# Optimization experiments

Hardware: AMD Instinct MI355X
Metric: run time of the kernel (lower is better)

Reference implementation:

```python
import jax, jax.numpy as jnp
import numpy as np

B, N, R, T, E, H, FE = 2, 512, 64, 128, 64, 8, 4
D = E // H  # head_dim = 8


def _layernorm(x, g, b):
    m = x.mean(-1, keepdims=True)
    v = ((x - m) ** 2).mean(-1, keepdims=True)
    return (x - m) / jnp.sqrt(v + 1e-5) * g + b


def _sattn(v, k, q, Wv, Wk, Wq, Wo, bo, mask):
    # v,k: (Bk,Nk,T,E); q: (Bq,Nq,T,E) with Bq possibly 1 (broadcast on batch)
    Bk, Nk, Tk, _ = v.shape
    Nq = q.shape[1]
    v = v.reshape(Bk, Nk, Tk, H, D) @ Wv
    k = k.reshape(Bk, Nk, Tk, H, D) @ Wk
    q = q.reshape(q.shape[0], Nq, Tk, H, D) @ Wq
    q = jnp.broadcast_to(q, (Bk, Nq, Tk, H, D))
    energy = jnp.einsum('bqthd,bkthd->bqkth', q, k)  # (B,Nq,Nk,T,H)
    if mask is not None:
        m = mask[None, :, :, None, None]
        energy = energy * m + (-1e8) * (1.0 - m)
    # note: non-standard softmax over the QUERY axis (dim=1), after scale+clamp
    att = jax.nn.softmax(jnp.clip(energy * (float(E) ** -0.5), -5.0, 5.0), axis=1)
    out = jnp.einsum('bqkth,bkthd->bqthd', att, v).reshape(Bk, Nq, Tk, E)
    return out @ Wo + bo, att


def setup_inputs() -> dict:
    rng = jax.random.key(0)
    ks = jax.random.split(rng, 40)
    s = 0.05
    inp = {
        'value': jax.random.normal(ks[0], (B, N, T, E), jnp.float32),
        'key': jax.random.normal(ks[1], (B, N, T, E), jnp.float32),
        'query': jax.random.normal(ks[2], (B, N, T, E), jnp.float32),
        'adj_sr': jax.random.randint(ks[3], (N, R), 0, 2).astype(jnp.int32),
        'adj_r': jax.random.randint(ks[4], (R, R), 0, 2).astype(jnp.int32),
        'D_S': jax.random.normal(ks[5], (N, R), jnp.float32) * s,
        'W_emb': jax.random.normal(ks[6], (R, E), jnp.float32) * s,
        'b_emb': jnp.zeros((E,), jnp.float32),
        'I_param': jax.random.normal(ks[7], (R, 1, E), jnp.float32) * s,
        'g1': jnp.ones((E,), jnp.float32), 'beta1': jnp.zeros((E,), jnp.float32),
        'g2': jnp.ones((E,), jnp.float32), 'beta2': jnp.zeros((E,), jnp.float32),
        'W_ff1': jax.random.normal(ks[8], (E, FE * E), jnp.float32) * s,
        'b_ff1': jnp.zeros((FE * E,), jnp.float32),
        'W_ff2': jax.random.normal(ks[9], (FE * E, E), jnp.float32) * s,
        'b_ff2': jnp.zeros((E,), jnp.float32),
        'W_fs': jax.random.normal(ks[10], (E, E), jnp.float32) * s,
        'b_fs': jnp.zeros((E,), jnp.float32),
    }
    i = 11
    for tag in ('sr', 'rr', 'rs'):
        inp['Wv_' + tag] = jax.random.normal(ks[i + 0], (D, D), jnp.float32) * s
        inp['Wk_' + tag] = jax.random.normal(ks[i + 1], (D, D), jnp.float32) * s
        inp['Wq_' + tag] = jax.random.normal(ks[i + 2], (D, D), jnp.float32) * s
        inp['Wo_' + tag] = jax.random.normal(ks[i + 3], (E, E), jnp.float32) * s
        inp['bo_' + tag] = jnp.zeros((E,), jnp.float32)
        i += 4
    return inp


def reference(value, key, query, adj_sr, adj_r, D_S, W_emb, b_emb, I_param,
              g1, beta1, g2, beta2, W_ff1, b_ff1, W_ff2, b_ff2, W_fs, b_fs,
              Wv_sr, Wk_sr, Wq_sr, Wo_sr, bo_sr,
              Wv_rr, Wk_rr, Wq_rr, Wo_rr, bo_rr,
              Wv_rs, Wk_rs, Wq_rs, Wo_rs, bo_rs):
    m_sr = adj_sr.T.astype(jnp.float32)  # (R,N)
    m_r = adj_r.astype(jnp.float32)      # (R,R)
    ds = D_S @ W_emb + b_emb             # (N,E)
    q = query + ds[None, :, None, :]
    k = key + ds[None, :, None, :]
    v = value
    Iq = jnp.broadcast_to(I_param[None], (1, R, T, E))  # I.repeat(1,1,T,1)
    Hh, asr = _sattn(v, k, Iq, Wv_sr, Wk_sr, Wq_sr, Wo_sr, bo_sr, m_sr)
    Hh, arr = _sattn(Hh, Hh, Hh, Wv_rr, Wk_rr, Wq_rr, Wo_rr, bo_rr, m_r)
    attn, ars = _sattn(Hh, Hh, q, Wv_rs, Wk_rs, Wq_rs, Wo_rs, bo_rs, None)
    x = _layernorm(attn + q, g1, beta1)          # dropout=0.0 -> identity
    ff = jax.nn.relu(x @ W_ff1 + b_ff1) @ W_ff2 + b_ff2
    U = _layernorm(ff + x, g2, beta2)
    out = U @ W_fs + b_fs
    return (out, asr, arr, ars, Hh)
```

## Files before the change

### kernel.cpp

```cpp
#include <hip/hip_runtime.h>
#include <hip/hip_bf16.h>

typedef __hip_bfloat16 bf16;

#define Bc 2
#define Nc 512
#define Rc 64
#define Tc 128
#define Ec 64
#define Hc 8
#define THc 1024
#define FFc 256

__device__ __forceinline__ bf16  f2b(float x){ return __float2bfloat16(x); }
__device__ __forceinline__ float us2f(unsigned short u){
  union { unsigned int i; float f; } c; c.i = ((unsigned int)u) << 16; return c.f;
}
__device__ __forceinline__ float clip5(float x){ return fminf(fmaxf(x, -5.0f), 5.0f); }

__device__ __forceinline__ float wave_sum64(float v){
#pragma unroll
  for (int o = 32; o > 0; o >>= 1) v += __shfl_xor(v, o, 64);
  return v;
}
__device__ __forceinline__ void wave_sum64x2(float& a, float& b){
#pragma unroll
  for (int o = 32; o > 0; o >>= 1){
    a += __shfl_xor(a, o, 64);
    b += __shfl_xor(b, o, 64);
  }
}

__device__ __forceinline__ float rowred16_sum(float v){
  v += __shfl_xor(v, 1, 64);
  v += __shfl_xor(v, 2, 64);
  v += __shfl_xor(v, 4, 64);
  v += __shfl_xor(v, 8, 64);
  return v;
}

__global__ __launch_bounds__(64) void k_prep(
    const float* __restrict__ DS, const float* __restrict__ Wemb,
    const float* __restrict__ bemb, const float* __restrict__ Ip,
    const float* __restrict__ Wq, float* __restrict__ ds, float* __restrict__ qhat)
{
  int bid = blockIdx.x, t = threadIdx.x;
  if (bid < Nc){
    int n = bid, e = t;
    __shared__ float row[Rc];
    row[t] = DS[n*Rc + t];
    __syncthreads();
    float acc = bemb[e];
    for (int r = 0; r < Rc; ++r) acc += row[r] * Wemb[r*Ec + e];
    ds[n*Ec + e] = acc;
  } else {
    int r = bid - Nc;
    __shared__ float irow[Ec];
    irow[t] = Ip[r*Ec + t];
    __syncthreads();
    int h = t >> 3, d = t & 7;
    float acc = 0.0f;
#pragma unroll
    for (int d0 = 0; d0 < 8; ++d0) acc += irow[h*8 + d0] * Wq[d0*8 + d];
    qhat[r*Ec + h*8 + d] = acc;
  }
}

__global__ __launch_bounds__(256) void k_proj_sr(
    const float* __restrict__ key, const float* __restrict__ value,
    const float* __restrict__ ds, const float* __restrict__ Wk,
    const float* __restrict__ Wv, float* __restrict__ khat, float* __restrict__ vhat)
{
  __shared__ float wk[64], wv[64];
  int t = threadIdx.x;
  if (t < 64){ wk[t] = Wk[t]; wv[t] = Wv[t]; }
  __syncthreads();
  int u = blockIdx.x*256 + t;
  int h = u & 7;
  int nt = u >> 3;
  int n = (nt / Tc) % Nc;
  const float* kp = key + (size_t)u*8;
  const float* vp = value + (size_t)u*8;
  const float* dsp = ds + n*Ec + h*8;
  float kin[8], vin[8];
#pragma unroll
  for (int d = 0; d < 8; ++d){ kin[d] = kp[d] + dsp[d]; vin[d] = vp[d]; }
  float* ko = khat + (size_t)u*8;
  float* vo = vhat + (size_t)u*8;
#pragma unroll
  for (int d = 0; d < 8; ++d){
    float ka = 0.0f, va = 0.0f;
#pragma unroll
    for (int d0 = 0; d0 < 8; ++d0){ ka += kin[d0]*wk[d0*8+d]; va += vin[d0]*wv[d0*8+d]; }
    ko[d] = ka; vo[d] = va;
  }
}

__global__ __launch_bounds__(256) void k_attn_sr(
    const float* __restrict__ khat, const float* __restrict__ vhat,
    const float* __restrict__ qhat, const int* __restrict__ adj_sr,
    float* __restrict__ pre)
{
  __shared__ float accs[4][64][8];
  int bid = blockIdx.x;
  int b = bid >> 10, th = bid & 1023;
  int t = th >> 3, h = th & 7;
  int tid = threadIdx.x;
  int r = tid & 63, w = tid >> 6;
  float q[8];
#pragma unroll
  for (int d = 0; d < 8; ++d) q[d] = qhat[r*Ec + h*8 + d];
  float acc[8] = {0,0,0,0,0,0,0,0};
  int n0 = w*128;
  for (int n = n0; n < n0 + 128; n += 2){
    size_t goA = ((size_t)((b*Nc + n)*Tc + t))*Ec + h*8;
    size_t goB = goA + (size_t)Tc*Ec;
    const float* kA = khat + goA;
    const float* kB = khat + goB;
    float eA = 0.0f, eB = 0.0f;
#pragma unroll
    for (int d = 0; d < 8; ++d){ eA += q[d]*kA[d]; eB += q[d]*kB[d]; }
    int mA = adj_sr[n*Rc + r], mB = adj_sr[(n+1)*Rc + r];
    eA = mA ? clip5(eA*0.125f) : -5.0f;
    eB = mB ? clip5(eB*0.125f) : -5.0f;
    float pA = __expf(eA), pB = __expf(eB);
    float sA = pA, sB = pB;
    wave_sum64x2(sA, sB);
    float aA = pA/sA, aB = pB/sB;
    const float* vA = vhat + goA;
    const float* vB = vhat + goB;
#pragma unroll
    for (int d = 0; d < 8; ++d) acc[d] += aA*vA[d] + aB*vB[d];
  }
#pragma unroll
  for (int d = 0; d < 8; ++d) accs[w][r][d] = acc[d];
  __syncthreads();
  if (w == 0){
    size_t po = ((size_t)((b*Rc + r)*Tc + t))*Ec + h*8;
#pragma unroll
    for (int d = 0; d < 8; ++d)
      pre[po + d] = accs[0][r][d] + accs[1][r][d] + accs[2][r][d] + accs[3][r][d];
  }
}

__global__ __launch_bounds__(256) void k_asr_write(
    const float* __restrict__ khat, const float* __restrict__ qhat,
    const int* __restrict__ adj_sr, float* __restrict__ o_asr)
{
  __shared__ float ql[4096];
  const float EXPM5 = 0.006737946999085467f;
  int bid = blockIdx.x;
  int b = bid >> 8, np = bid & 255;
  int tid = threadIdx.x;
  int n = np*2 + (tid >> 7);
  int t = tid & 127;
#pragma unroll
  for (int i = 0; i < 16; ++i) ql[i*256 + tid] = qhat[i*256 + tid];
  __syncthreads();
  const float* kp = khat + ((size_t)((b*Nc + n)*Tc + t))*Ec;
  float kr[64];
#pragma unroll
  for (int i = 0; i < 16; ++i) *(float4*)&kr[i*4] = *(const float4*)&kp[i*4];

  float s[8] = {0,0,0,0,0,0,0,0};
  for (int r = 0; r < 64; ++r){
    int m = adj_sr[n*Rc + r];
    if (m){
      const float* qr = &ql[r*64];
#pragma unroll
      for (int h = 0; h < 8; ++h){
        float4 qa = *(const float4*)&qr[h*8];
        float4 qb = *(const float4*)&qr[h*8 + 4];
        float e = qa.x*kr[h*8+0] + qa.y*kr[h*8+1] + qa.z*kr[h*8+2] + qa.w*kr[h*8+3]
                + qb.x*kr[h*8+4] + qb.y*kr[h*8+5] + qb.z*kr[h*8+6] + qb.w*kr[h*8+7];
        s[h] += __expf(clip5(e*0.125f));
      }
    } else {
#pragma unroll
      for (int h = 0; h < 8; ++h) s[h] += EXPM5;
    }
  }
  float rs_[8];
#pragma unroll
  for (int h = 0; h < 8; ++h) rs_[h] = __builtin_amdgcn_rcpf(s[h]);

  for (int r = 0; r < 64; ++r){
    int m = adj_sr[n*Rc + r];
    float a[8];
    if (m){
      const float* qr = &ql[r*64];
#pragma unroll
      for (int h = 0; h < 8; ++h){
        float4 qa = *(const float4*)&qr[h*8];
        float4 qb = *(const float4*)&qr[h*8 + 4];
        float e = qa.x*kr[h*8+0] + qa.y*kr[h*8+1] + qa.z*kr[h*8+2] + qa.w*kr[h*8+3]
                + qb.x*kr[h*8+4] + qb.y*kr[h*8+5] + qb.z*kr[h*8+6] + qb.w*kr[h*8+7];
        a[h] = __expf(clip5(e*0.125f)) * rs_[h];
      }
    } else {
#pragma unroll
      for (int h = 0; h < 8; ++h) a[h] = EXPM5 * rs_[h];
    }
    size_t ao = ((size_t)((b*Rc + r)*Nc + n))*THc + t*8;
    *(float4*)&o_asr[ao]     = make_float4(a[0], a[1], a[2], a[3]);
    *(float4*)&o_asr[ao + 4] = make_float4(a[4], a[5], a[6], a[7]);
  }
}

__global__ __launch_bounds__(256) void k_attn_rr(
    const float* __restrict__ qh, const float* __restrict__ kh,
    const float* __restrict__ vh, const int* __restrict__ adj_r,
    bf16* __restrict__ att_c, float* __restrict__ pre)
{
  __shared__ float accs[4][64][8];
  int bid = blockIdx.x;
  int b = bid >> 10, th = bid & 1023;
  int t = th >> 3, h = th & 7;
  int tid = threadIdx.x;
  int q = tid & 63, w = tid >> 6;
  size_t qo = ((size_t)((b*Rc + q)*Tc + t))*Ec + h*8;
  float qv[8];
#pragma unroll
  for (int d = 0; d < 8; ++d) qv[d] = qh[qo + d];
  float acc[8] = {0,0,0,0,0,0,0,0};
  int k0 = w*16;
  for (int k = k0; k < k0 + 16; k += 2){
    size_t koA = ((size_t)((b*Rc + k)*Tc + t))*Ec + h*8;
    size_t koB = koA + (size_t)Tc*Ec;
    const float* kA = kh + koA;
    const float* kB = kh + koB;
    float eA = 0.0f, eB = 0.0f;
#pragma unroll
    for (int d = 0; d < 8; ++d){ eA += qv[d]*kA[d]; eB += qv[d]*kB[d]; }
    int mA = adj_r[q*Rc + k], mB = adj_r[q*Rc + k + 1];
    eA = mA ? clip5(eA*0.125f) : -5.0f;
    eB = mB ? clip5(eB*0.125f) : -5.0f;
    float pA = __expf(eA), pB = __expf(eB);
    float sA = pA, sB = pB;
    wave_sum64x2(sA, sB);
    float aA = pA/sA, aB = pB/sB;
    size_t ao = ((size_t)(b*Rc + k)*THc + th)*Rc + q;
    att_c[ao] = f2b(aA);
    att_c[ao + (size_t)THc*Rc] = f2b(aB);
    const float* vA = vh + koA;
    const float* vB = vh + koB;
#pragma unroll
    for (int d = 0; d < 8; ++d) acc[d] += aA*vA[d] + aB*vB[d];
  }
#pragma unroll
  for (int d = 0; d < 8; ++d) accs[w][q][d] = acc[d];
  __syncthreads();
  if (w == 0){
#pragma unroll
    for (int d = 0; d < 8; ++d)
      pre[qo + d] = accs[0][q][d] + accs[1][q][d] + accs[2][q][d] + accs[3][q][d];
  }
}

__global__ __launch_bounds__(512) void k_attn_rs(
    const float* __restrict__ query, const float* __restrict__ ds,
    const float* __restrict__ Wq, const float* __restrict__ kh,
    const float* __restrict__ vh, bf16* __restrict__ att_c, float* __restrict__ pre)
{
  __shared__ float wq[64];
  __shared__ float kl[64][8];
  __shared__ float vl[64][8];
  __shared__ float redS[2][2][8];
  int bid = blockIdx.x;
  int b = bid >> 10, th = bid & 1023;
  int t = th >> 3, h = th & 7;
  int q = threadIdx.x;
  if (q < 64) wq[q] = Wq[q];
  {
    int kk = q >> 3, d = q & 7;
    size_t o = ((size_t)((b*Rc + kk)*Tc + t))*Ec + h*8 + d;
    kl[kk][d] = kh[o];
    vl[kk][d] = vh[o];
  }
  __syncthreads();
  size_t qro = ((size_t)((b*Nc + q)*Tc + t))*Ec + h*8;
  const float* dsp = ds + q*Ec + h*8;
  float xin[8], qv[8];
#pragma unroll
  for (int d = 0; d < 8; ++d) xin[d] = query[qro + d] + dsp[d];
#pragma unroll
  for (int d = 0; d < 8; ++d){
    float a = 0.0f;
#pragma unroll
    for (int d0 = 0; d0 < 8; ++d0) a += xin[d0]*wq[d0*8 + d];
    qv[d] = a;
  }
  float acc[8] = {0,0,0,0,0,0,0,0};
  int lane = q & 63, wv = q >> 6;
  for (int k = 0; k < 64; k += 2){
    float eA = 0.0f, eB = 0.0f;
#pragma unroll
    for (int d = 0; d < 8; ++d){ eA += qv[d]*kl[k][d]; eB += qv[d]*kl[k+1][d]; }
    eA = clip5(eA*0.125f);
    eB = clip5(eB*0.125f);
    float pA = __expf(eA), pB = __expf(eB);
    float sA = pA, sB = pB;
    wave_sum64x2(sA, sB);
    int pb = (k >> 1) & 1;
    if (lane == 0){ redS[pb][0][wv] = sA; redS[pb][1][wv] = sB; }
    __syncthreads();
    float stA = 0.0f, stB = 0.0f;
#pragma unroll
    for (int i = 0; i < 8; ++i){ stA += redS[pb][0][i]; stB += redS[pb][1][i]; }
    float aA = pA/stA, aB = pB/stB;
    size_t ao = ((size_t)(b*Rc + k)*THc + th)*Nc + q;
    att_c[ao] = f2b(aA);
    att_c[ao + (size_t)THc*Nc] = f2b(aB);
#pragma unroll
    for (int d = 0; d < 8; ++d) acc[d] += aA*vl[k][d] + aB*vl[k+1][d];
  }
#pragma unroll
  for (int d = 0; d < 8; ++d) pre[qro + d] = acc[d];
}

__global__ __launch_bounds__(256) void k_transpose(
    const unsigned short* __restrict__ src, float* __restrict__ dst,
    int W, int C)
{
  __shared__ unsigned short tile[64][66];
  int bid = blockIdx.x;
  int nct = C >> 6;
  int ct = bid % nct; bid /= nct;
  int tht = bid & 15; bid >>= 4;
  int w = bid % W; int b = bid / W;
  int tt = threadIdx.x;
  {
    int cs = tt & 63, i0 = tt >> 6;
    const unsigned short* sb = src + ((size_t)(b*W + w)*THc + tht*64)*C + ct*64;
#pragma unroll
    for (int p = 0; p < 16; ++p){
      int i = i0 + p*4;
      tile[i][cs] = sb[(size_t)i*C + cs];
    }
  }
  __syncthreads();
  {
    int i = tt & 63, c0 = tt >> 6;
#pragma unroll
    for (int p = 0; p < 16; ++p){
      int cs = c0 + p*4;
      int c = ct*64 + cs;
      dst[((size_t)(b*C + c)*W + w)*THc + tht*64 + i] = us2f(tile[i][cs]);
    }
  }
}

__global__ __launch_bounds__(256) void k_wo(
    const float* __restrict__ pre, int nparts, int pstride,
    const float* __restrict__ Wo,
    const float* __restrict__ bo, float* __restrict__ outf,
    float* __restrict__ outf2, int nrows)
{
  int gt = blockIdx.x*256 + threadIdx.x;
  int row = gt >> 6, lane = gt & 63;
  if (row >= nrows) return;
  float xin = 0.0f;
  for (int p2 = 0; p2 < nparts; ++p2)
    xin += pre[(size_t)p2*pstride + (size_t)row*64 + lane];
  float acc = bo[lane];
  for (int e = 0; e < 64; ++e){
    float xe = __shfl(xin, e, 64);
    acc += xe * Wo[e*64 + lane];
  }
  outf[(size_t)row*64 + lane] = acc;
  if (outf2) outf2[(size_t)row*64 + lane] = acc;
}

__global__ __launch_bounds__(256) void k_proj3(
    const float* __restrict__ src, const float* Wq, const float* Wk, const float* Wv,
    float* qh, float* kh, float* vh, int nunits)
{
  __shared__ float wq[64], wk[64], wv[64];
  int t = threadIdx.x;
  if (t < 64){
    wq[t] = Wq ? Wq[t] : 0.0f;
    wk[t] = Wk[t];
    wv[t] = Wv[t];
  }
  __syncthreads();
  int u = blockIdx.x*256 + t;
  if (u >= nunits) return;
  const float* sp = src + (size_t)u*8;
  float xin[8];
#pragma unroll
  for (int d = 0; d < 8; ++d) xin[d] = sp[d];
#pragma unroll
  for (int d = 0; d < 8; ++d){
    float qa = 0.0f, ka = 0.0f, va = 0.0f;
#pragma unroll
    for (int d0 = 0; d0 < 8; ++d0){
      qa += xin[d0]*wq[d0*8 + d];
      ka += xin[d0]*wk[d0*8 + d];
      va += xin[d0]*wv[d0*8 + d];
    }
    if (qh) qh[(size_t)u*8 + d] = qa;
    kh[(size_t)u*8 + d] = ka;
    vh[(size_t)u*8 + d] = va;
  }
}

__device__ __forceinline__ void gemm64x64(
    const float (* __restrict__ Xs)[68], const float* __restrict__ W,
    int Wld, int r0, int c0, float acc[4][4])
{
#pragma unroll 4
  for (int k = 0; k < 64; k += 4){
    float4 xr0 = *(const float4*)&Xs[r0+0][k];
    float4 xr1 = *(const float4*)&Xs[r0+1][k];
    float4 xr2 = *(const float4*)&Xs[r0+2][k];
    float4 xr3 = *(const float4*)&Xs[r0+3][k];
#pragma unroll
    for (int kk = 0; kk < 4; ++kk){
      float4 w = *(const float4*)&W[(size_t)(k+kk)*Wld + c0];
      float x0 = (&xr0.x)[kk], x1 = (&xr1.x)[kk];
      float x2 = (&xr2.x)[kk], x3 = (&xr3.x)[kk];
      acc[0][0] += x0*w.x; acc[0][1] += x0*w.y; acc[0][2] += x0*w.z; acc[0][3] += x0*w.w;
      acc[1][0] += x1*w.x; acc[1][1] += x1*w.y; acc[1][2] += x1*w.z; acc[1][3] += x1*w.w;
      acc[2][0] += x2*w.x; acc[2][1] += x2*w.y; acc[2][2] += x2*w.z; acc[2][3] += x2*w.w;
      acc[3][0] += x3*w.x; acc[3][1] += x3*w.y; acc[3][2] += x3*w.z; acc[3][3] += x3*w.w;
    }
  }
}

__device__ __forceinline__ void ln64(
    const float acc[4][4], float4 g, float4 b, float out[4][4])
{
#pragma unroll
  for (int i = 0; i < 4; ++i){
    float s = acc[i][0] + acc[i][1] + acc[i][2] + acc[i][3];
    float m = rowred16_sum(s) * (1.0f/64.0f);
    float d0 = acc[i][0] - m, d1 = acc[i][1] - m, d2 = acc[i][2] - m, d3 = acc[i][3] - m;
    float vv = d0*d0 + d1*d1 + d2*d2 + d3*d3;
    float var = rowred16_sum(vv) * (1.0f/64.0f);
    float rs = rsqrtf(var + 1e-5f);
    out[i][0] = d0*rs*g.x + b.x;
    out[i][1] = d1*rs*g.y + b.y;
    out[i][2] = d2*rs*g.z + b.z;
    out[i][3] = d3*rs*g.w + b.w;
  }
}

__global__ __launch_bounds__(256) void k_tail(
    const float* __restrict__ pre3, const float* __restrict__ query,
    const float* __restrict__ ds,
    const float* __restrict__ Wo, const float* __restrict__ bo,
    const float* __restrict__ g1, const float* __restrict__ be1,
    const float* __restrict__ W1, const float* __restrict__ b1,
    const float* __restrict__ W2, const float* __restrict__ b2,
    const float* __restrict__ g2, const float* __restrict__ be2,
    const float* __restrict__ Wfs, const float* __restrict__ bfs,
    float* __restrict__ outp)
{
  __shared__ float Xs[64][68];
  __shared__ float Hs[64][68];
  int tid = threadIdx.x;
  int cg = tid & 15, rg = tid >> 4;
  int r0 = rg*4, c0 = cg*4;
  int row_base = blockIdx.x * 64;
  int n = (row_base >> 7) & (Nc - 1);

#pragma unroll
  for (int i = 0; i < 4; ++i){
    float4 t = *(const float4*)&pre3[(size_t)(row_base + r0 + i)*64 + c0];
    *(float4*)&Xs[r0+i][c0] = t;
  }

  float4 bo4  = *(const float4*)&bo[c0];
  float4 ds4  = *(const float4*)&ds[n*64 + c0];
  float4 g14  = *(const float4*)&g1[c0];
  float4 be14 = *(const float4*)&be1[c0];
  float4 b24  = *(const float4*)&b2[c0];
  float4 g24  = *(const float4*)&g2[c0];
  float4 be24 = *(const float4*)&be2[c0];
  float4 bfs4 = *(const float4*)&bfs[c0];
  __syncthreads();

  float acc[4][4];
#pragma unroll
  for (int i = 0; i < 4; ++i){
    acc[i][0] = bo4.x; acc[i][1] = bo4.y; acc[i][2] = bo4.z; acc[i][3] = bo4.w;
  }
  gemm64x64(Xs, Wo, 64, r0, c0, acc);
#pragma unroll
  for (int i = 0; i < 4; ++i){
    float4 qv = *(const float4*)&query[(size_t)(row_base + r0 + i)*64 + c0];
    acc[i][0] += qv.x + ds4.x;
    acc[i][1] += qv.y + ds4.y;
    acc[i][2] += qv.z + ds4.z;
    acc[i][3] += qv.w + ds4.w;
  }
  float xt[4][4];
  ln64(acc, g14, be14, xt);
  __syncthreads();
#pragma unroll
  for (int i = 0; i < 4; ++i)
    *(float4*)&Xs[r0+i][c0] = make_float4(xt[i][0], xt[i][1], xt[i][2], xt[i][3]);
  __syncthreads();

  float ff[4][4];
#pragma unroll
  for (int i = 0; i < 4; ++i){
    ff[i][0] = b24.x; ff[i][1] = b24.y; ff[i][2] = b24.z; ff[i][3] = b24.w;
  }
  for (int p = 0; p < 4; ++p){
    float4 b14 = *(const float4*)&b1[p*64 + c0];
    float h[4][4];
#pragma unroll
    for (int i = 0; i < 4; ++i){
      h[i][0] = b14.x; h[i][1] = b14.y; h[i][2] = b14.z; h[i][3] = b14.w;
    }
    gemm64x64(Xs, W1 + p*64, 256, r0, c0, h);
#pragma unroll
    for (int i = 0; i < 4; ++i){
      h[i][0] = fmaxf(h[i][0], 0.0f); h[i][1] = fmaxf(h[i][1], 0.0f);
      h[i][2] = fmaxf(h[i][2], 0.0f); h[i][3] = fmaxf(h[i][3], 0.0f);
    }
    __syncthreads();
#pragma unroll
    for (int i = 0; i < 4; ++i)
      *(float4*)&Hs[r0+i][c0] = make_float4(h[i][0], h[i][1], h[i][2], h[i][3]);
    __syncthreads();
    gemm64x64(Hs, W2 + (size_t)p*64*64, 64, r0, c0, ff);
  }

#pragma unroll
  for (int i = 0; i < 4; ++i){
    float4 xv = *(const float4*)&Xs[r0+i][c0];
    ff[i][0] += xv.x; ff[i][1] += xv.y; ff[i][2] += xv.z; ff[i][3] += xv.w;
  }
  float U[4][4];
  ln64(ff, g24, be24, U);
  __syncthreads();
#pragma unroll
  for (int i = 0; i < 4; ++i)
    *(float4*)&Hs[r0+i][c0] = make_float4(U[i][0], U[i][1], U[i][2], U[i][3]);
  __syncthreads();

  float o[4][4];
#pragma unroll
  for (int i = 0; i < 4; ++i){
    o[i][0] = bfs4.x; o[i][1] = bfs4.y; o[i][2] = bfs4.z; o[i][3] = bfs4.w;
  }
  gemm64x64(Hs, Wfs, 64, r0, c0, o);
#pragma unroll
  for (int i = 0; i < 4; ++i)
    *(float4*)&outp[(size_t)(row_base + r0 + i)*64 + c0] =
        make_float4(o[i][0], o[i][1], o[i][2], o[i][3]);
}

extern "C" void kernel_launch(void* const* d_in, const int* in_sizes, int n_in,
                              void* d_out, int out_size, void* d_ws, size_t ws_size,
                              hipStream_t stream)
{
  const float* value = (const float*)d_in[0];
  const float* key   = (const float*)d_in[1];
  const float* query = (const float*)d_in[2];
  const int*  adj_sr = (const int*)d_in[3];
  const int*  adj_r  = (const int*)d_in[4];
  const float* D_S   = (const float*)d_in[5];
  const float* W_emb = (const float*)d_in[6];
  const float* b_emb = (const float*)d_in[7];
  const float* I_par = (const float*)d_in[8];
  const float* g1    = (const float*)d_in[9];
  const float* be1   = (const float*)d_in[10];
  const float* g2    = (const float*)d_in[11];
  const float* be2   = (const float*)d_in[12];
  const float* W_ff1 = (const float*)d_in[13];
  const float* b_ff1 = (const float*)d_in[14];
  const float* W_ff2 = (const float*)d_in[15];
  const float* b_ff2 = (const float*)d_in[16];
  const float* W_fs  = (const float*)d_in[17];
  const float* b_fs  = (const float*)d_in[18];
  const float* Wv_sr = (const float*)d_in[19];
  const float* Wk_sr = (const float*)d_in[20];
  const float* Wq_sr = (const float*)d_in[21];
  const float* Wo_sr = (const float*)d_in[22];
  const float* bo_sr = (const float*)d_in[23];
  const float* Wv_rr = (const float*)d_in[24];
  const float* Wk_rr = (const float*)d_in[25];
  const float* Wq_rr = (const float*)d_in[26];
  const float* Wo_rr = (const float*)d_in[27];
  const float* bo_rr = (const float*)d_in[28];
  const float* Wv_rs = (const float*)d_in[29];
  const float* Wk_rs = (const float*)d_in[30];
  const float* Wq_rs = (const float*)d_in[31];
  const float* Wo_rs = (const float*)d_in[32];
  const float* bo_rs = (const float*)d_in[33];

  float* outp  = (float*)d_out;
  float* o_out = outp;
  float* o_asr = outp + 8388608;
  float* o_arr = outp + 75497472;
  float* o_ars = outp + 83886080;
  float* o_hh  = outp + 150994944;

  float* wsf = (float*)d_ws;
  float* ws_ds   = wsf;
  float* ws_qsr  = wsf + 32768;
  bf16*  ws_att  = (bf16*)(wsf + 36864);
  float* pool    = wsf + 36864 + 33554432;
  float* ws_ksr  = pool;
  float* ws_vsr  = pool + 8388608;
  float* ws_pre1 = pool + 16777216;
  float* ws_hh1  = pool + 17825792;
  float* ws_qrr  = pool;
  float* ws_krr  = pool + 1048576;
  float* ws_vrr  = pool + 2097152;
  float* ws_pre2 = pool + 3145728;
  float* ws_hh2  = pool + 4194304;
  float* ws_krs  = pool + 5242880;
  float* ws_vrs  = pool + 6291456;
  float* ws_pre3 = pool + 7340032;

  k_prep<<<576, 64, 0, stream>>>(D_S, W_emb, b_emb, I_par, Wq_sr, ws_ds, ws_qsr);
  k_proj_sr<<<4096, 256, 0, stream>>>(key, value, ws_ds, Wk_sr, Wv_sr, ws_ksr, ws_vsr);
  k_attn_sr<<<2048, 256, 0, stream>>>(ws_ksr, ws_vsr, ws_qsr, adj_sr, ws_pre1);
  k_asr_write<<<512, 256, 0, stream>>>(ws_ksr, ws_qsr, adj_sr, o_asr);
  k_wo<<<4096, 256, 0, stream>>>(ws_pre1, 1, 0, Wo_sr, bo_sr,
                                 ws_hh1, (float*)nullptr, 16384);

  k_proj3<<<512, 256, 0, stream>>>(ws_hh1, Wq_rr, Wk_rr, Wv_rr,
                                   ws_qrr, ws_krr, ws_vrr, 131072);
  k_attn_rr<<<2048, 256, 0, stream>>>(ws_qrr, ws_krr, ws_vrr, adj_r, ws_att, ws_pre2);
  k_transpose<<<2048, 256, 0, stream>>>((const unsigned short*)ws_att, o_arr, 64, 64);
  k_wo<<<4096, 256, 0, stream>>>(ws_pre2, 1, 0, Wo_rr, bo_rr, ws_hh2, o_hh, 16384);

  k_proj3<<<512, 256, 0, stream>>>(ws_hh2, (const float*)nullptr, Wk_rs, Wv_rs,
                                   (float*)nullptr, ws_krs, ws_vrs, 131072);
  k_attn_rs<<<2048, 512, 0, stream>>>(query, ws_ds, Wq_rs, ws_krs, ws_vrs,
                                      ws_att, ws_pre3);
  k_transpose<<<16384, 256, 0, stream>>>((const unsigned short*)ws_att, o_ars, 64, 512);

  k_tail<<<2048, 256, 0, stream>>>(ws_pre3, query, ws_ds, Wo_rs, bo_rs,
                                   g1, be1, W_ff1, b_ff1, W_ff2, b_ff2,
                                   g2, be2, W_fs, b_fs, o_out);
}
```

Measured before the change: 848.2 us.

## Recompute rs attention probabilities directly into output instead of bf16 staging plus transpose

```diff
diff --git a/kernel.cpp b/kernel.cpp
--- a/kernel.cpp
+++ b/kernel.cpp
@@ -96,10 +96,80 @@
   }
 }
 
+__global__ __launch_bounds__(256) void k_asr_write(
+    const float* __restrict__ khat, const float* __restrict__ qhat,
+    const int* __restrict__ adj_sr, float* __restrict__ o_asr,
+    float* __restrict__ rDsr)
+{
+  __shared__ float ql[4096];
+  const float EXPM5 = 0.006737946999085467f;
+  int bid = blockIdx.x;
+  int b = bid >> 8, np = bid & 255;
+  int tid = threadIdx.x;
+  int n = np*2 + (tid >> 7);
+  int t = tid & 127;
+#pragma unroll
+  for (int i = 0; i < 16; ++i) ql[i*256 + tid] = qhat[i*256 + tid];
+  __syncthreads();
+  const float* kp = khat + ((size_t)((b*Nc + n)*Tc + t))*Ec;
+  float kr[64];
+#pragma unroll
+  for (int i = 0; i < 16; ++i) *(float4*)&kr[i*4] = *(const float4*)&kp[i*4];
+
+  float s[8] = {0,0,0,0,0,0,0,0};
+  for (int r = 0; r < 64; ++r){
+    int m = adj_sr[n*Rc + r];
+    if (m){
+      const float* qr = &ql[r*64];
+#pragma unroll
+      for (int h = 0; h < 8; ++h){
+        float4 qa = *(const float4*)&qr[h*8];
+        float4 qb = *(const float4*)&qr[h*8 + 4];
+        float e = qa.x*kr[h*8+0] + qa.y*kr[h*8+1] + qa.z*kr[h*8+2] + qa.w*kr[h*8+3]
+                + qb.x*kr[h*8+4] + qb.y*kr[h*8+5] + qb.z*kr[h*8+6] + qb.w*kr[h*8+7];
+        s[h] += __expf(clip5(e*0.125f));
+      }
+    } else {
+#pragma unroll
+      for (int h = 0; h < 8; ++h) s[h] += EXPM5;
+    }
+  }
+  float rs_[8];
+#pragma unroll
+  for (int h = 0; h < 8; ++h) rs_[h] = __builtin_amdgcn_rcpf(s[h]);
+  {
+    size_t dbase = ((size_t)((b*Nc + n)*Tc + t))*8;
+    *(float4*)&rDsr[dbase]     = make_float4(rs_[0], rs_[1], rs_[2], rs_[3]);
+    *(float4*)&rDsr[dbase + 4] = make_float4(rs_[4], rs_[5], rs_[6], rs_[7]);
+  }
+
+  for (int r = 0; r < 64; ++r){
+    int m = adj_sr[n*Rc + r];
+    float a[8];
+    if (m){
+      const float* qr = &ql[r*64];
+#pragma unroll
+      for (int h = 0; h < 8; ++h){
+        float4 qa = *(const float4*)&qr[h*8];
+        float4 qb = *(const float4*)&qr[h*8 + 4];
+        float e = qa.x*kr[h*8+0] + qa.y*kr[h*8+1] + qa.z*kr[h*8+2] + qa.w*kr[h*8+3]
+                + qb.x*kr[h*8+4] + qb.y*kr[h*8+5] + qb.z*kr[h*8+6] + qb.w*kr[h*8+7];
+        a[h] = __expf(clip5(e*0.125f)) * rs_[h];
+      }
+    } else {
+#pragma unroll
+      for (int h = 0; h < 8; ++h) a[h] = EXPM5 * rs_[h];
+    }
+    size_t ao = ((size_t)((b*Rc + r)*Nc + n))*THc + t*8;
+    *(float4*)&o_asr[ao]     = make_float4(a[0], a[1], a[2], a[3]);
+    *(float4*)&o_asr[ao + 4] = make_float4(a[4], a[5], a[6], a[7]);
+  }
+}
+
 __global__ __launch_bounds__(256) void k_attn_sr(
     const float* __restrict__ khat, const float* __restrict__ vhat,
     const float* __restrict__ qhat, const int* __restrict__ adj_sr,
-    float* __restrict__ pre)
+    const float* __restrict__ rD, float* __restrict__ pre)
 {
   __shared__ float accs[4][64][8];
   int bid = blockIdx.x;
@@ -123,10 +193,10 @@
     int mA = adj_sr[n*Rc + r], mB = adj_sr[(n+1)*Rc + r];
     eA = mA ? clip5(eA*0.125f) : -5.0f;
     eB = mB ? clip5(eB*0.125f) : -5.0f;
-    float pA = __expf(eA), pB = __expf(eB);
-    float sA = pA, sB = pB;
-    wave_sum64x2(sA, sB);
-    float aA = pA/sA, aB = pB/sB;
+    float rdA = rD[((size_t)((b*Nc + n  )*Tc + t))*8 + h];
+    float rdB = rD[((size_t)((b*Nc + n+1)*Tc + t))*8 + h];
+    float aA = __expf(eA) * rdA;
+    float aB = __expf(eB) * rdB;
     const float* vA = vhat + goA;
     const float* vB = vhat + goB;
 #pragma unroll
@@ -140,70 +210,6 @@
 #pragma unroll
     for (int d = 0; d < 8; ++d)
       pre[po + d] = accs[0][r][d] + accs[1][r][d] + accs[2][r][d] + accs[3][r][d];
-  }
-}
-
-__global__ __launch_bounds__(256) void k_asr_write(
-    const float* __restrict__ khat, const float* __restrict__ qhat,
-    const int* __restrict__ adj_sr, float* __restrict__ o_asr)
-{
-  __shared__ float ql[4096];
-  const float EXPM5 = 0.006737946999085467f;
-  int bid = blockIdx.x;
-  int b = bid >> 8, np = bid & 255;
-  int tid = threadIdx.x;
-  int n = np*2 + (tid >> 7);
-  int t = tid & 127;
-#pragma unroll
-  for (int i = 0; i < 16; ++i) ql[i*256 + tid] = qhat[i*256 + tid];
-  __syncthreads();
-  const float* kp = khat + ((size_t)((b*Nc + n)*Tc + t))*Ec;
-  float kr[64];
-#pragma unroll
-  for (int i = 0; i < 16; ++i) *(float4*)&kr[i*4] = *(const float4*)&kp[i*4];
-
-  float s[8] = {0,0,0,0,0,0,0,0};
-  for (int r = 0; r < 64; ++r){
-    int m = adj_sr[n*Rc + r];
-    if (m){
-      const float* qr = &ql[r*64];
-#pragma unroll
-      for (int h = 0; h < 8; ++h){
-        float4 qa = *(const float4*)&qr[h*8];
-        float4 qb = *(const float4*)&qr[h*8 + 4];
-        float e = qa.x*kr[h*8+0] + qa.y*kr[h*8+1] + qa.z*kr[h*8+2] + qa.w*kr[h*8+3]
-                + qb.x*kr[h*8+4] + qb.y*kr[h*8+5] + qb.z*kr[h*8+6] + qb.w*kr[h*8+7];
-        s[h] += __expf(clip5(e*0.125f));
-      }
-    } else {
-#pragma unroll
-      for (int h = 0; h < 8; ++h) s[h] += EXPM5;
-    }
-  }
-  float rs_[8];
-#pragma unroll
-  for (int h = 0; h < 8; ++h) rs_[h] = __builtin_amdgcn_rcpf(s[h]);
-
-  for (int r = 0; r < 64; ++r){
-    int m = adj_sr[n*Rc + r];
-    float a[8];
-    if (m){
-      const float* qr = &ql[r*64];
-#pragma unroll
-      for (int h = 0; h < 8; ++h){
-        float4 qa = *(const float4*)&qr[h*8];
-        float4 qb = *(const float4*)&qr[h*8 + 4];
-        float e = qa.x*kr[h*8+0] + qa.y*kr[h*8+1] + qa.z*kr[h*8+2] + qa.w*kr[h*8+3]
-                + qb.x*kr[h*8+4] + qb.y*kr[h*8+5] + qb.z*kr[h*8+6] + qb.w*kr[h*8+7];
-        a[h] = __expf(clip5(e*0.125f)) * rs_[h];
-      }
-    } else {
-#pragma unroll
-      for (int h = 0; h < 8; ++h) a[h] = EXPM5 * rs_[h];
-    }
-    size_t ao = ((size_t)((b*Rc + r)*Nc + n))*THc + t*8;
-    *(float4*)&o_asr[ao]     = make_float4(a[0], a[1], a[2], a[3]);
-    *(float4*)&o_asr[ao + 4] = make_float4(a[4], a[5], a[6], a[7]);
   }
 }
 
@@ -260,7 +266,8 @@
 __global__ __launch_bounds__(512) void k_attn_rs(
     const float* __restrict__ query, const float* __restrict__ ds,
     const float* __restrict__ Wq, const float* __restrict__ kh,
-    const float* __restrict__ vh, bf16* __restrict__ att_c, float* __restrict__ pre)
+    const float* __restrict__ vh, float* __restrict__ rDrs,
+    float* __restrict__ pre)
 {
   __shared__ float wq[64];
   __shared__ float kl[64][8];
@@ -307,15 +314,72 @@
     float stA = 0.0f, stB = 0.0f;
 #pragma unroll
     for (int i = 0; i < 8; ++i){ stA += redS[pb][0][i]; stB += redS[pb][1][i]; }
+    if (q == 0){
+      rDrs[((size_t)((b*Rc + k  )*Tc + t))*8 + h] = __builtin_amdgcn_rcpf(stA);
+      rDrs[((size_t)((b*Rc + k+1)*Tc + t))*8 + h] = __builtin_amdgcn_rcpf(stB);
+    }
     float aA = pA/stA, aB = pB/stB;
-    size_t ao = ((size_t)(b*Rc + k)*THc + th)*Nc + q;
-    att_c[ao] = f2b(aA);
-    att_c[ao + (size_t)THc*Nc] = f2b(aB);
 #pragma unroll
     for (int d = 0; d < 8; ++d) acc[d] += aA*vl[k][d] + aB*vl[k+1][d];
   }
 #pragma unroll
   for (int d = 0; d < 8; ++d) pre[qro + d] = acc[d];
+}
+
+__global__ __launch_bounds__(512) void k_ars_write(
+    const float* __restrict__ query, const float* __restrict__ ds,
+    const float* __restrict__ Wq, const float* __restrict__ kh,
+    const float* __restrict__ rD, float* __restrict__ o_ars)
+{
+  __shared__ float wq[64];
+  int bid = blockIdx.x;
+  int b = bid >> 7, qc = bid & 127;
+  int tid = threadIdx.x;
+  int t = tid & 127, ql = tid >> 7;
+  int q = qc*4 + ql;
+  if (tid < 64) wq[tid] = Wq[tid];
+  __syncthreads();
+  size_t qro = ((size_t)((b*Nc + q)*Tc + t))*Ec;
+  float xin[64];
+#pragma unroll
+  for (int i = 0; i < 16; ++i){
+    float4 v = *(const float4*)&query[qro + i*4];
+    float4 dv = *(const float4*)&ds[q*Ec + i*4];
+    xin[i*4+0] = v.x + dv.x;
+    xin[i*4+1] = v.y + dv.y;
+    xin[i*4+2] = v.z + dv.z;
+    xin[i*4+3] = v.w + dv.w;
+  }
+  float qv[64];
+#pragma unroll
+  for (int h = 0; h < 8; ++h){
+#pragma unroll
+    for (int d = 0; d < 8; ++d){
+      float a = 0.0f;
+#pragma unroll
+      for (int d0 = 0; d0 < 8; ++d0) a += xin[h*8 + d0]*wq[d0*8 + d];
+      qv[h*8 + d] = a;
+    }
+  }
+  for (int k = 0; k < 64; ++k){
+    size_t kro = ((size_t)((b*Rc + k)*Tc + t))*Ec;
+    const float* kp = kh + kro;
+    float4 rd0 = *(const float4*)&rD[((size_t)((b*Rc + k)*Tc + t))*8];
+    float4 rd1 = *(const float4*)&rD[((size_t)((b*Rc + k)*Tc + t))*8 + 4];
+    float a[8];
+#pragma unroll
+    for (int h = 0; h < 8; ++h){
+      float e = 0.0f;
+#pragma unroll
+      for (int d = 0; d < 8; ++d) e += qv[h*8 + d]*kp[h*8 + d];
+      a[h] = __expf(clip5(e*0.125f));
+    }
+    a[0] *= rd0.x; a[1] *= rd0.y; a[2] *= rd0.z; a[3] *= rd0.w;
+    a[4] *= rd1.x; a[5] *= rd1.y; a[6] *= rd1.z; a[7] *= rd1.w;
+    size_t ao = ((size_t)((b*Nc + q)*Rc + k))*THc + t*8;
+    *(float4*)&o_ars[ao]     = make_float4(a[0], a[1], a[2], a[3]);
+    *(float4*)&o_ars[ao + 4] = make_float4(a[4], a[5], a[6], a[7]);
+  }
 }
 
 __global__ __launch_bounds__(256) void k_transpose(
@@ -602,7 +666,9 @@
   float* wsf = (float*)d_ws;
   float* ws_ds   = wsf;
   float* ws_qsr  = wsf + 32768;
-  bf16*  ws_att  = (bf16*)(wsf + 36864);
+  float* ws_rDsr = wsf + 36864;
+  bf16*  ws_att  = (bf16*)(wsf + 36864 + 1048576);
+  float* ws_rDrs = wsf + 36864 + 1048576 + 4194304;
   float* pool    = wsf + 36864 + 33554432;
   float* ws_ksr  = pool;
   float* ws_vsr  = pool + 8388608;
@@ -619,8 +685,9 @@
 
   k_prep<<<576, 64, 0, stream>>>(D_S, W_emb, b_emb, I_par, Wq_sr, ws_ds, ws_qsr);
   k_proj_sr<<<4096, 256, 0, stream>>>(key, value, ws_ds, Wk_sr, Wv_sr, ws_ksr, ws_vsr);
-  k_attn_sr<<<2048, 256, 0, stream>>>(ws_ksr, ws_vsr, ws_qsr, adj_sr, ws_pre1);
-  k_asr_write<<<512, 256, 0, stream>>>(ws_ksr, ws_qsr, adj_sr, o_asr);
+  k_asr_write<<<512, 256, 0, stream>>>(ws_ksr, ws_qsr, adj_sr, o_asr, ws_rDsr);
+  k_attn_sr<<<2048, 256, 0, stream>>>(ws_ksr, ws_vsr, ws_qsr, adj_sr,
+                                      ws_rDsr, ws_pre1);
   k_wo<<<4096, 256, 0, stream>>>(ws_pre1, 1, 0, Wo_sr, bo_sr,
                                  ws_hh1, (float*)nullptr, 16384);
 
@@ -633,8 +700,9 @@
   k_proj3<<<512, 256, 0, stream>>>(ws_hh2, (const float*)nullptr, Wk_rs, Wv_rs,
                                    (float*)nullptr, ws_krs, ws_vrs, 131072);
   k_attn_rs<<<2048, 512, 0, stream>>>(query, ws_ds, Wq_rs, ws_krs, ws_vrs,
-                                      ws_att, ws_pre3);
-  k_transpose<<<16384, 256, 0, stream>>>((const unsigned short*)ws_att, o_ars, 64, 512);
+                                      ws_rDrs, ws_pre3);
+  k_ars_write<<<256, 512, 0, stream>>>(query, ws_ds, Wq_rs, ws_krs,
+                                       ws_rDrs, o_ars);
 
   k_tail<<<2048, 256, 0, stream>>>(ws_pre3, query, ws_ds, Wo_rs, bo_rs,
                                    g1, be1, W_ff1, b_ff1, W_ff2, b_ff2,
```

Result: slower. 1.035 ms (+22.0%).

## Reuse precomputed softmax denominators in sr attention and batch rs reductions

Applied to the files above, without the earlier changes.

```diff
diff --git a/kernel.cpp b/kernel.cpp
--- a/kernel.cpp
+++ b/kernel.cpp
@@ -28,6 +28,15 @@
   for (int o = 32; o > 0; o >>= 1){
     a += __shfl_xor(a, o, 64);
     b += __shfl_xor(b, o, 64);
+  }
+}
+__device__ __forceinline__ void wave_sum64x4(float& a, float& b, float& c, float& d){
+#pragma unroll
+  for (int o = 32; o > 0; o >>= 1){
+    a += __shfl_xor(a, o, 64);
+    b += __shfl_xor(b, o, 64);
+    c += __shfl_xor(c, o, 64);
+    d += __shfl_xor(d, o, 64);
   }
 }
 
@@ -96,20 +105,94 @@
   }
 }
 
+__global__ __launch_bounds__(256) void k_asr_write(
+    const float* __restrict__ khat, const float* __restrict__ qhat,
+    const int* __restrict__ adj_sr, float* __restrict__ o_asr,
+    float* __restrict__ rDsr)
+{
+  __shared__ float ql[4096];
+  const float EXPM5 = 0.006737946999085467f;
+  int bid = blockIdx.x;
+  int b = bid >> 8, np = bid & 255;
+  int tid = threadIdx.x;
+  int n = np*2 + (tid >> 7);
+  int t = tid & 127;
+#pragma unroll
+  for (int i = 0; i < 16; ++i) ql[i*256 + tid] = qhat[i*256 + tid];
+  __syncthreads();
+  const float* kp = khat + ((size_t)((b*Nc + n)*Tc + t))*Ec;
+  float kr[64];
+#pragma unroll
+  for (int i = 0; i < 16; ++i) *(float4*)&kr[i*4] = *(const float4*)&kp[i*4];
+
+  float s[8] = {0,0,0,0,0,0,0,0};
+  for (int r = 0; r < 64; ++r){
+    int m = adj_sr[n*Rc + r];
+    if (m){
+      const float* qr = &ql[r*64];
+#pragma unroll
+      for (int h = 0; h < 8; ++h){
+        float4 qa = *(const float4*)&qr[h*8];
+        float4 qb = *(const float4*)&qr[h*8 + 4];
+        float e = qa.x*kr[h*8+0] + qa.y*kr[h*8+1] + qa.z*kr[h*8+2] + qa.w*kr[h*8+3]
+                + qb.x*kr[h*8+4] + qb.y*kr[h*8+5] + qb.z*kr[h*8+6] + qb.w*kr[h*8+7];
+        s[h] += __expf(clip5(e*0.125f));
+      }
+    } else {
+#pragma unroll
+      for (int h = 0; h < 8; ++h) s[h] += EXPM5;
+    }
+  }
+  float rs_[8];
+#pragma unroll
+  for (int h = 0; h < 8; ++h) rs_[h] = __builtin_amdgcn_rcpf(s[h]);
+  {
+    size_t dbase = ((size_t)((b*Nc + n)*Tc + t))*8;
+    *(float4*)&rDsr[dbase]     = make_float4(rs_[0], rs_[1], rs_[2], rs_[3]);
+    *(float4*)&rDsr[dbase + 4] = make_float4(rs_[4], rs_[5], rs_[6], rs_[7]);
+  }
+
+  for (int r = 0; r < 64; ++r){
+    int m = adj_sr[n*Rc + r];
+    float a[8];
+    if (m){
+      const float* qr = &ql[r*64];
+#pragma unroll
+      for (int h = 0; h < 8; ++h){
+        float4 qa = *(const float4*)&qr[h*8];
+        float4 qb = *(const float4*)&qr[h*8 + 4];
+        float e = qa.x*kr[h*8+0] + qa.y*kr[h*8+1] + qa.z*kr[h*8+2] + qa.w*kr[h*8+3]
+                + qb.x*kr[h*8+4] + qb.y*kr[h*8+5] + qb.z*kr[h*8+6] + qb.w*kr[h*8+7];
+        a[h] = __expf(clip5(e*0.125f)) * rs_[h];
+      }
+    } else {
+#pragma unroll
+      for (int h = 0; h < 8; ++h) a[h] = EXPM5 * rs_[h];
+    }
+    size_t ao = ((size_t)((b*Rc + r)*Nc + n))*THc + t*8;
+    *(float4*)&o_asr[ao]     = make_float4(a[0], a[1], a[2], a[3]);
+    *(float4*)&o_asr[ao + 4] = make_float4(a[4], a[5], a[6], a[7]);
+  }
+}
+
 __global__ __launch_bounds__(256) void k_attn_sr(
     const float* __restrict__ khat, const float* __restrict__ vhat,
     const float* __restrict__ qhat, const int* __restrict__ adj_sr,
-    float* __restrict__ pre)
+    const float* __restrict__ rD, float* __restrict__ pre)
 {
   __shared__ float accs[4][64][8];
+  __shared__ float rDl[512];
   int bid = blockIdx.x;
   int b = bid >> 10, th = bid & 1023;
   int t = th >> 3, h = th & 7;
   int tid = threadIdx.x;
   int r = tid & 63, w = tid >> 6;
+  rDl[tid]       = rD[((size_t)((b*Nc + tid      )*Tc + t))*8 + h];
+  rDl[tid + 256] = rD[((size_t)((b*Nc + tid + 256)*Tc + t))*8 + h];
   float q[8];
 #pragma unroll
   for (int d = 0; d < 8; ++d) q[d] = qhat[r*Ec + h*8 + d];
+  __syncthreads();
   float acc[8] = {0,0,0,0,0,0,0,0};
   int n0 = w*128;
   for (int n = n0; n < n0 + 128; n += 2){
@@ -123,10 +206,8 @@
     int mA = adj_sr[n*Rc + r], mB = adj_sr[(n+1)*Rc + r];
     eA = mA ? clip5(eA*0.125f) : -5.0f;
     eB = mB ? clip5(eB*0.125f) : -5.0f;
-    float pA = __expf(eA), pB = __expf(eB);
-    float sA = pA, sB = pB;
-    wave_sum64x2(sA, sB);
-    float aA = pA/sA, aB = pB/sB;
+    float aA = __expf(eA) * rDl[n];
+    float aB = __expf(eB) * rDl[n+1];
     const float* vA = vhat + goA;
     const float* vB = vhat + goB;
 #pragma unroll
@@ -140,70 +221,6 @@
 #pragma unroll
     for (int d = 0; d < 8; ++d)
       pre[po + d] = accs[0][r][d] + accs[1][r][d] + accs[2][r][d] + accs[3][r][d];
-  }
-}
-
-__global__ __launch_bounds__(256) void k_asr_write(
-    const float* __restrict__ khat, const float* __restrict__ qhat,
-    const int* __restrict__ adj_sr, float* __restrict__ o_asr)
-{
-  __shared__ float ql[4096];
-  const float EXPM5 = 0.006737946999085467f;
-  int bid = blockIdx.x;
-  int b = bid >> 8, np = bid & 255;
-  int tid = threadIdx.x;
-  int n = np*2 + (tid >> 7);
-  int t = tid & 127;
-#pragma unroll
-  for (int i = 0; i < 16; ++i) ql[i*256 + tid] = qhat[i*256 + tid];
-  __syncthreads();
-  const float* kp = khat + ((size_t)((b*Nc + n)*Tc + t))*Ec;
-  float kr[64];
-#pragma unroll
-  for (int i = 0; i < 16; ++i) *(float4*)&kr[i*4] = *(const float4*)&kp[i*4];
-
-  float s[8] = {0,0,0,0,0,0,0,0};
-  for (int r = 0; r < 64; ++r){
-    int m = adj_sr[n*Rc + r];
-    if (m){
-      const float* qr = &ql[r*64];
-#pragma unroll
-      for (int h = 0; h < 8; ++h){
-        float4 qa = *(const float4*)&qr[h*8];
-        float4 qb = *(const float4*)&qr[h*8 + 4];
-        float e = qa.x*kr[h*8+0] + qa.y*kr[h*8+1] + qa.z*kr[h*8+2] + qa.w*kr[h*8+3]
-                + qb.x*kr[h*8+4] + qb.y*kr[h*8+5] + qb.z*kr[h*8+6] + qb.w*kr[h*8+7];
-        s[h] += __expf(clip5(e*0.125f));
-      }
-    } else {
-#pragma unroll
-      for (int h = 0; h < 8; ++h) s[h] += EXPM5;
-    }
-  }
-  float rs_[8];
-#pragma unroll
-  for (int h = 0; h < 8; ++h) rs_[h] = __builtin_amdgcn_rcpf(s[h]);
-
-  for (int r = 0; r < 64; ++r){
-    int m = adj_sr[n*Rc + r];
-    float a[8];
-    if (m){
-      const float* qr = &ql[r*64];
-#pragma unroll
-      for (int h = 0; h < 8; ++h){
-        float4 qa = *(const float4*)&qr[h*8];
-        float4 qb = *(const float4*)&qr[h*8 + 4];
-        float e = qa.x*kr[h*8+0] + qa.y*kr[h*8+1] + qa.z*kr[h*8+2] + qa.w*kr[h*8+3]
-                + qb.x*kr[h*8+4] + qb.y*kr[h*8+5] + qb.z*kr[h*8+6] + qb.w*kr[h*8+7];
-        a[h] = __expf(clip5(e*0.125f)) * rs_[h];
-      }
-    } else {
-#pragma unroll
-      for (int h = 0; h < 8; ++h) a[h] = EXPM5 * rs_[h];
-    }
-    size_t ao = ((size_t)((b*Rc + r)*Nc + n))*THc + t*8;
-    *(float4*)&o_asr[ao]     = make_float4(a[0], a[1], a[2], a[3]);
-    *(float4*)&o_asr[ao + 4] = make_float4(a[4], a[5], a[6], a[7]);
   }
 }
 
@@ -265,7 +282,8 @@
   __shared__ float wq[64];
   __shared__ float kl[64][8];
   __shared__ float vl[64][8];
-  __shared__ float redS[2][2][8];
+  __shared__ float part[8][64];
+  __shared__ float redr[64];
   int bid = blockIdx.x;
   int b = bid >> 10, th = bid & 1023;
   int t = th >> 3, h = th & 7;
@@ -290,24 +308,40 @@
     for (int d0 = 0; d0 < 8; ++d0) a += xin[d0]*wq[d0*8 + d];
     qv[d] = a;
   }
+  int lane = q & 63, wv = q >> 6;
+  for (int k = 0; k < 64; k += 4){
+    float s0 = 0.0f, s1 = 0.0f, s2 = 0.0f, s3 = 0.0f;
+#pragma unroll
+    for (int d = 0; d < 8; ++d){
+      s0 += qv[d]*kl[k  ][d];
+      s1 += qv[d]*kl[k+1][d];
+      s2 += qv[d]*kl[k+2][d];
+      s3 += qv[d]*kl[k+3][d];
+    }
+    s0 = __expf(clip5(s0*0.125f));
+    s1 = __expf(clip5(s1*0.125f));
+    s2 = __expf(clip5(s2*0.125f));
+    s3 = __expf(clip5(s3*0.125f));
+    wave_sum64x4(s0, s1, s2, s3);
+    if (lane == 0){
+      part[wv][k] = s0; part[wv][k+1] = s1; part[wv][k+2] = s2; part[wv][k+3] = s3;
+    }
+  }
+  __syncthreads();
+  if (q < 64){
+    float s = 0.0f;
+#pragma unroll
+    for (int w2 = 0; w2 < 8; ++w2) s += part[w2][q];
+    redr[q] = __builtin_amdgcn_rcpf(s);
+  }
+  __syncthreads();
   float acc[8] = {0,0,0,0,0,0,0,0};
-  int lane = q & 63, wv = q >> 6;
   for (int k = 0; k < 64; k += 2){
     float eA = 0.0f, eB = 0.0f;
 #pragma unroll
     for (int d = 0; d < 8; ++d){ eA += qv[d]*kl[k][d]; eB += qv[d]*kl[k+1][d]; }
-    eA = clip5(eA*0.125f);
-    eB = clip5(eB*0.125f);
-    float pA = __expf(eA), pB = __expf(eB);
-    float sA = pA, sB = pB;
-    wave_sum64x2(sA, sB);
-    int pb = (k >> 1) & 1;
-    if (lane == 0){ redS[pb][0][wv] = sA; redS[pb][1][wv] = sB; }
-    __syncthreads();
-    float stA = 0.0f, stB = 0.0f;
-#pragma unroll
-    for (int i = 0; i < 8; ++i){ stA += redS[pb][0][i]; stB += redS[pb][1][i]; }
-    float aA = pA/stA, aB = pB/stB;
+    float aA = __expf(clip5(eA*0.125f)) * redr[k];
+    float aB = __expf(clip5(eB*0.125f)) * redr[k+1];
     size_t ao = ((size_t)(b*Rc + k)*THc + th)*Nc + q;
     att_c[ao] = f2b(aA);
     att_c[ao + (size_t)THc*Nc] = f2b(aB);
@@ -603,6 +637,7 @@
   float* ws_ds   = wsf;
   float* ws_qsr  = wsf + 32768;
   bf16*  ws_att  = (bf16*)(wsf + 36864);
+  float* ws_rDsr = wsf + 36864;
   float* pool    = wsf + 36864 + 33554432;
   float* ws_ksr  = pool;
   float* ws_vsr  = pool + 8388608;
@@ -619,8 +654,9 @@
 
   k_prep<<<576, 64, 0, stream>>>(D_S, W_emb, b_emb, I_par, Wq_sr, ws_ds, ws_qsr);
   k_proj_sr<<<4096, 256, 0, stream>>>(key, value, ws_ds, Wk_sr, Wv_sr, ws_ksr, ws_vsr);
-  k_attn_sr<<<2048, 256, 0, stream>>>(ws_ksr, ws_vsr, ws_qsr, adj_sr, ws_pre1);
-  k_asr_write<<<512, 256, 0, stream>>>(ws_ksr, ws_qsr, adj_sr, o_asr);
+  k_asr_write<<<512, 256, 0, stream>>>(ws_ksr, ws_qsr, adj_sr, o_asr, ws_rDsr);
+  k_attn_sr<<<2048, 256, 0, stream>>>(ws_ksr, ws_vsr, ws_qsr, adj_sr,
+                                      ws_rDsr, ws_pre1);
   k_wo<<<4096, 256, 0, stream>>>(ws_pre1, 1, 0, Wo_sr, bo_sr,
                                  ws_hh1, (float*)nullptr, 16384);
 
```

New measurement: 855.2 us. Within noise of the previous version (+0.8%).
